# Performance work log

Measured on AMD Instinct MI355X. Metric: run time of the kernel, lower is better.

Reference implementation:

```python
import jax, jax.numpy as jnp
import numpy as np

N = 262144
D = 256
G = 2048

def setup_inputs() -> dict:
    key = jax.random.key(0)
    k1, k2, k3, k4, k5, k6 = jax.random.split(key, 6)
    x = jax.random.normal(k1, (N, D), dtype=jnp.float32)
    batch = jnp.sort(jax.random.randint(k2, (N,), 0, G, dtype=jnp.int32))
    # attention_net params: Linear(D, D//2) -> ReLU -> Linear(D//2, 1)
    s1 = 1.0 / np.sqrt(D)
    s2 = 1.0 / np.sqrt(D // 2)
    W1 = jax.random.uniform(k3, (D, D // 2), jnp.float32, -s1, s1)
    b1 = jax.random.uniform(k4, (D // 2,), jnp.float32, -s1, s1)
    W2 = jax.random.uniform(k5, (D // 2, 1), jnp.float32, -s2, s2)
    b2 = jax.random.uniform(k6, (1,), jnp.float32, -s2, s2)
    return {"x": x, "batch": batch, "num_graphs": G, "W1": W1, "b1": b1, "W2": W2, "b2": b2}

def reference(x, batch, num_graphs, W1, b1, W2, b2):
    # attention scores: [N, 1]
    h = jax.nn.relu(x @ W1 + b1)
    scores = (h @ W2 + b2)[:, 0]  # [N]
    # segment softmax over nodes of each graph (stable)
    seg_max = jax.ops.segment_max(scores, batch, num_segments=num_graphs)  # [G]
    ex = jnp.exp(scores - seg_max[batch])
    seg_sum = jax.ops.segment_sum(ex, batch, num_segments=num_graphs)  # [G]
    weights = ex / seg_sum[batch]  # [N]
    # weighted scatter-add pooling -> [G, D]
    graph_features = jax.ops.segment_sum(x * weights[:, None], batch, num_segments=num_graphs)
    return graph_features
```

## Files before the change

kernel.cpp:

```cpp
#include <hip/hip_runtime.h>
#include <hip/hip_bf16.h>

#define NN 262144
#define DD 256
#define HH 128
#define GG 2048

typedef __attribute__((ext_vector_type(8))) __bf16 bf16x8;
typedef __attribute__((ext_vector_type(4))) float f32x4;

union ABFrag { bf16x8 v; unsigned short u[8]; };
union BFrag  { bf16x8 v; uint4 i; };

__device__ __forceinline__ unsigned short f2bf(float f) {
    unsigned int u = __float_as_uint(f);
    unsigned int r = (u + 0x7fffu + ((u >> 16) & 1u)) >> 16;
    return (unsigned short)r;
}

__global__ void prep_kernel(const float* __restrict__ w1, unsigned short* __restrict__ w1t) {
    int i = blockIdx.x * 256 + threadIdx.x;
    int n = i >> 8;
    int k = i & 255;
    w1t[i] = f2bf(w1[k * HH + n]);
}

__global__ __launch_bounds__(256, 2)
void scores_kernel(const float* __restrict__ x,
                   const unsigned short* __restrict__ w1t,
                   const float* __restrict__ b1,
                   const float* __restrict__ w2,
                   const float* __restrict__ b2,
                   float* __restrict__ scores)
{
    const int lane = threadIdx.x & 63;
    const int wv   = threadIdx.x >> 6;
    const int c = lane & 15;
    const int q = lane >> 4;
    const int rowBlock = blockIdx.x * 256 + wv * 64;

    float b1v[8], w2v[8];
#pragma unroll
    for (int t = 0; t < 8; ++t) { b1v[t] = b1[t * 16 + c]; w2v[t] = w2[t * 16 + c]; }
    const float b2s = b2[0];

    f32x4 acc[4][8];
#pragma unroll
    for (int it = 0; it < 4; ++it)
#pragma unroll
        for (int t = 0; t < 8; ++t) acc[it][t] = (f32x4){0.f, 0.f, 0.f, 0.f};

#pragma unroll
    for (int kk = 0; kk < 8; ++kk) {
        BFrag bf[8];
#pragma unroll
        for (int t = 0; t < 8; ++t) {
            const uint4* p = (const uint4*)(w1t + (size_t)(t * 16 + c) * DD + kk * 32 + q * 8);
            bf[t].i = *p;
        }
#pragma unroll
        for (int it = 0; it < 4; ++it) {
            const float* px = x + (size_t)(rowBlock + it * 16 + c) * DD + kk * 32 + q * 8;
            float4 f0 = *(const float4*)px;
            float4 f1 = *(const float4*)(px + 4);
            ABFrag af;
            af.u[0] = f2bf(f0.x); af.u[1] = f2bf(f0.y); af.u[2] = f2bf(f0.z); af.u[3] = f2bf(f0.w);
            af.u[4] = f2bf(f1.x); af.u[5] = f2bf(f1.y); af.u[6] = f2bf(f1.z); af.u[7] = f2bf(f1.w);
#pragma unroll
            for (int t = 0; t < 8; ++t)
                acc[it][t] = __builtin_amdgcn_mfma_f32_16x16x32_bf16(af.v, bf[t].v, acc[it][t], 0, 0, 0);
        }
    }

#pragma unroll
    for (int it = 0; it < 4; ++it) {
        float s0 = 0.f, s1 = 0.f, s2 = 0.f, s3 = 0.f;
#pragma unroll
        for (int t = 0; t < 8; ++t) {
            float w = w2v[t], bb = b1v[t];
            f32x4 a = acc[it][t];
            s0 += fmaxf(a.x + bb, 0.f) * w;
            s1 += fmaxf(a.y + bb, 0.f) * w;
            s2 += fmaxf(a.z + bb, 0.f) * w;
            s3 += fmaxf(a.w + bb, 0.f) * w;
        }
#pragma unroll
        for (int off = 1; off < 16; off <<= 1) {
            s0 += __shfl_xor(s0, off);
            s1 += __shfl_xor(s1, off);
            s2 += __shfl_xor(s2, off);
            s3 += __shfl_xor(s3, off);
        }
        if (c == 0) {
            float* o = scores + rowBlock + it * 16 + q * 4;
            o[0] = s0 + b2s; o[1] = s1 + b2s; o[2] = s2 + b2s; o[3] = s3 + b2s;
        }
    }
}

__global__ void stats_kernel(const float* __restrict__ scores,
                             const int* __restrict__ batch,
                             float* __restrict__ gmax, float* __restrict__ ginv,
                             int* __restrict__ bstart, int* __restrict__ bend)
{
    int g = blockIdx.x;
    int lo = 0, hi = NN;
    while (lo < hi) { int mid = (lo + hi) >> 1; if (batch[mid] < g) lo = mid + 1; else hi = mid; }
    int start = lo;
    hi = NN;
    while (lo < hi) { int mid = (lo + hi) >> 1; if (batch[mid] < g + 1) lo = mid + 1; else hi = mid; }
    int end = lo;

    int lane = threadIdx.x;
    float m = -3.402823466e38f;
    for (int i = start + lane; i < end; i += 64) m = fmaxf(m, scores[i]);
#pragma unroll
    for (int off = 1; off < 64; off <<= 1) m = fmaxf(m, __shfl_xor(m, off));
    float sum = 0.f;
    for (int i = start + lane; i < end; i += 64) sum += __expf(scores[i] - m);
#pragma unroll
    for (int off = 1; off < 64; off <<= 1) sum += __shfl_xor(sum, off);
    if (lane == 0) {
        gmax[g] = m;
        ginv[g] = (end > start) ? 1.0f / sum : 0.0f;
        bstart[g] = start;
        bend[g] = end;
    }
}

__global__ __launch_bounds__(256)
void pool_kernel(const float* __restrict__ x, const float* __restrict__ scores,
                 const float* __restrict__ gmax, const float* __restrict__ ginv,
                 const int* __restrict__ bstart, const int* __restrict__ bend,
                 float* __restrict__ out)
{
    int g = blockIdx.x;
    int d = threadIdx.x;
    int start = bstart[g], end = bend[g];
    float m = gmax[g], inv = ginv[g];
    __shared__ float wl[256];
    float acc = 0.f;
    for (int base = start; base < end; base += 256) {
        int nch = min(256, end - base);
        __syncthreads();
        if (d < nch) wl[d] = __expf(scores[base + d] - m) * inv;
        __syncthreads();
        int j = 0;
        for (; j + 4 <= nch; j += 4) {
            const float* px = x + (size_t)(base + j) * DD + d;
            float x0 = px[0], x1 = px[DD], x2 = px[2 * DD], x3 = px[3 * DD];
            acc = fmaf(wl[j], x0, acc);
            acc = fmaf(wl[j + 1], x1, acc);
            acc = fmaf(wl[j + 2], x2, acc);
            acc = fmaf(wl[j + 3], x3, acc);
        }
        for (; j < nch; ++j) acc = fmaf(wl[j], x[(size_t)(base + j) * DD + d], acc);
    }
    out[(size_t)g * DD + d] = acc;
}

extern "C" void kernel_launch(void* const* d_in, const int* in_sizes, int n_in,
                              void* d_out, int out_size, void* d_ws, size_t ws_size,
                              hipStream_t stream) {
    const float* x     = (const float*)d_in[0];
    const int*   batch = (const int*)d_in[1];
    const float* W1    = (const float*)d_in[3];
    const float* b1    = (const float*)d_in[4];
    const float* W2    = (const float*)d_in[5];
    const float* b2    = (const float*)d_in[6];
    float* out = (float*)d_out;

    char* ws = (char*)d_ws;
    float*          scores = (float*)ws;
    unsigned short* w1t    = (unsigned short*)(ws + (size_t)NN * 4);
    float*          gmax   = (float*)(ws + (size_t)NN * 4 + 65536);
    float*          ginv   = gmax + GG;
    int*            bstart = (int*)(ginv + GG);
    int*            bend   = bstart + GG;

    prep_kernel<<<HH * DD / 256, 256, 0, stream>>>(W1, w1t);
    scores_kernel<<<NN / 256, 256, 0, stream>>>(x, w1t, b1, W2, b2, scores);
    stats_kernel<<<GG, 64, 0, stream>>>(scores, batch, gmax, ginv, bstart, bend);
    pool_kernel<<<GG, 256, 0, stream>>>(x, scores, gmax, ginv, bstart, bend, out);
}
```

Measured before the change: 433.5 us.

## Fuse score MLP, online segment softmax and pooling into one per-graph kernel

Replaces the separate scores, stats and pool kernels with a single kernel per graph. Each block stages W1 (bf16) in padded LDS, computes scores for 64-row chunks with MFMA, maintains an online softmax (running max and sum with rescaling), and accumulates the weighted pooling from the same rows, which are likely still in cache. Segment bounds come from a small separate binary-search kernel. This removes the scores round trip and the second full pass over x, but it adds three block barriers per 64-row chunk, lowers parallelism to one block per graph with about 68KB of LDS each, and repeats the W1 LDS load in every block. b2 is dropped because a constant shift cancels in the softmax.

```diff
diff --git a/kernel.cpp b/kernel.cpp
--- a/kernel.cpp
+++ b/kernel.cpp
@@ -5,17 +5,16 @@
 #define DD 256
 #define HH 128
 #define GG 2048
+#define LW1 264
 
 typedef __attribute__((ext_vector_type(8))) __bf16 bf16x8;
 typedef __attribute__((ext_vector_type(4))) float f32x4;
 
-union ABFrag { bf16x8 v; unsigned short u[8]; };
-union BFrag  { bf16x8 v; uint4 i; };
+union ABFrag { bf16x8 v; unsigned short u[8]; uint4 i; };
 
 __device__ __forceinline__ unsigned short f2bf(float f) {
     unsigned int u = __float_as_uint(f);
-    unsigned int r = (u + 0x7fffu + ((u >> 16) & 1u)) >> 16;
-    return (unsigned short)r;
+    return (unsigned short)((u + 0x7fffu + ((u >> 16) & 1u)) >> 16);
 }
 
 __global__ void prep_kernel(const float* __restrict__ w1, unsigned short* __restrict__ w1t) {
@@ -25,60 +24,88 @@
     w1t[i] = f2bf(w1[k * HH + n]);
 }
 
+__global__ void bounds_kernel(const int* __restrict__ batch, int* __restrict__ bnd) {
+    int g = blockIdx.x * 256 + threadIdx.x;
+    if (g > GG) return;
+    int lo = 0, hi = NN;
+    while (lo < hi) { int mid = (lo + hi) >> 1; if (batch[mid] < g) lo = mid + 1; else hi = mid; }
+    bnd[g] = lo;
+}
+
 __global__ __launch_bounds__(256, 2)
-void scores_kernel(const float* __restrict__ x,
-                   const unsigned short* __restrict__ w1t,
-                   const float* __restrict__ b1,
-                   const float* __restrict__ w2,
-                   const float* __restrict__ b2,
-                   float* __restrict__ scores)
+void fused_kernel(const float* __restrict__ x,
+                  const unsigned short* __restrict__ w1t,
+                  const float* __restrict__ b1,
+                  const float* __restrict__ w2,
+                  const int* __restrict__ bnd,
+                  float* __restrict__ out)
 {
-    const int lane = threadIdx.x & 63;
-    const int wv   = threadIdx.x >> 6;
+    __shared__ __align__(16) unsigned short w1s[HH * LW1];
+    __shared__ float s_lds[64];
+    __shared__ float e_lds[64];
+    __shared__ float bc[2];
+
+    const int g = blockIdx.x;
+    const int tid = threadIdx.x;
+    const int lane = tid & 63;
+    const int wv = tid >> 6;
     const int c = lane & 15;
     const int q = lane >> 4;
-    const int rowBlock = blockIdx.x * 256 + wv * 64;
+
+    const int start = bnd[g];
+    const int end = bnd[g + 1];
+
+#pragma unroll
+    for (int k = 0; k < 16; ++k) {
+        int idx = tid + k * 256;
+        int r = idx >> 5;
+        int col = (idx & 31) * 8;
+        *(uint4*)&w1s[r * LW1 + col] = ((const uint4*)w1t)[idx];
+    }
 
     float b1v[8], w2v[8];
 #pragma unroll
     for (int t = 0; t < 8; ++t) { b1v[t] = b1[t * 16 + c]; w2v[t] = w2[t * 16 + c]; }
-    const float b2s = b2[0];
 
-    f32x4 acc[4][8];
+    __syncthreads();
+
+    float acc = 0.f;
+    float m = -3.402823466e38f;
+    float l = 0.f;
+
+    for (int base = start; base < end; base += 64) {
+        f32x4 accs[8];
 #pragma unroll
-    for (int it = 0; it < 4; ++it)
-#pragma unroll
-        for (int t = 0; t < 8; ++t) acc[it][t] = (f32x4){0.f, 0.f, 0.f, 0.f};
+        for (int t = 0; t < 8; ++t) accs[t] = (f32x4){0.f, 0.f, 0.f, 0.f};
+
+        const int row = base + wv * 16 + c;
+        const bool valid = row < end;
+        const float* px = x + (size_t)row * DD;
 
 #pragma unroll
-    for (int kk = 0; kk < 8; ++kk) {
-        BFrag bf[8];
+        for (int kk = 0; kk < 8; ++kk) {
+            ABFrag af;
+            if (valid) {
+                float4 f0 = *(const float4*)(px + kk * 32 + q * 8);
+                float4 f1 = *(const float4*)(px + kk * 32 + q * 8 + 4);
+                af.u[0] = f2bf(f0.x); af.u[1] = f2bf(f0.y); af.u[2] = f2bf(f0.z); af.u[3] = f2bf(f0.w);
+                af.u[4] = f2bf(f1.x); af.u[5] = f2bf(f1.y); af.u[6] = f2bf(f1.z); af.u[7] = f2bf(f1.w);
+            } else {
+                af.i = (uint4){0u, 0u, 0u, 0u};
+            }
 #pragma unroll
-        for (int t = 0; t < 8; ++t) {
-            const uint4* p = (const uint4*)(w1t + (size_t)(t * 16 + c) * DD + kk * 32 + q * 8);
-            bf[t].i = *p;
+            for (int t = 0; t < 8; ++t) {
+                ABFrag bf;
+                bf.i = *(const uint4*)&w1s[(t * 16 + c) * LW1 + kk * 32 + q * 8];
+                accs[t] = __builtin_amdgcn_mfma_f32_16x16x32_bf16(af.v, bf.v, accs[t], 0, 0, 0);
+            }
         }
-#pragma unroll
-        for (int it = 0; it < 4; ++it) {
-            const float* px = x + (size_t)(rowBlock + it * 16 + c) * DD + kk * 32 + q * 8;
-            float4 f0 = *(const float4*)px;
-            float4 f1 = *(const float4*)(px + 4);
-            ABFrag af;
-            af.u[0] = f2bf(f0.x); af.u[1] = f2bf(f0.y); af.u[2] = f2bf(f0.z); af.u[3] = f2bf(f0.w);
-            af.u[4] = f2bf(f1.x); af.u[5] = f2bf(f1.y); af.u[6] = f2bf(f1.z); af.u[7] = f2bf(f1.w);
-#pragma unroll
-            for (int t = 0; t < 8; ++t)
-                acc[it][t] = __builtin_amdgcn_mfma_f32_16x16x32_bf16(af.v, bf[t].v, acc[it][t], 0, 0, 0);
-        }
-    }
 
-#pragma unroll
-    for (int it = 0; it < 4; ++it) {
         float s0 = 0.f, s1 = 0.f, s2 = 0.f, s3 = 0.f;
 #pragma unroll
         for (int t = 0; t < 8; ++t) {
             float w = w2v[t], bb = b1v[t];
-            f32x4 a = acc[it][t];
+            f32x4 a = accs[t];
             s0 += fmaxf(a.x + bb, 0.f) * w;
             s1 += fmaxf(a.y + bb, 0.f) * w;
             s2 += fmaxf(a.z + bb, 0.f) * w;
@@ -92,71 +119,45 @@
             s3 += __shfl_xor(s3, off);
         }
         if (c == 0) {
-            float* o = scores + rowBlock + it * 16 + q * 4;
-            o[0] = s0 + b2s; o[1] = s1 + b2s; o[2] = s2 + b2s; o[3] = s3 + b2s;
+            float* o = s_lds + wv * 16 + q * 4;
+            o[0] = s0; o[1] = s1; o[2] = s2; o[3] = s3;
         }
+        __syncthreads();
+
+        if (wv == 0) {
+            const int n = min(64, end - base);
+            float s = (lane < n) ? s_lds[lane] : -3.402823466e38f;
+            float cmax = s;
+#pragma unroll
+            for (int off = 1; off < 64; off <<= 1) cmax = fmaxf(cmax, __shfl_xor(cmax, off));
+            float newm = fmaxf(m, cmax);
+            float alpha = __expf(m - newm);
+            float e = (lane < n) ? __expf(s - newm) : 0.f;
+            float es = e;
+#pragma unroll
+            for (int off = 1; off < 64; off <<= 1) es += __shfl_xor(es, off);
+            l = l * alpha + es;
+            m = newm;
+            e_lds[lane] = e;
+            if (lane == 0) bc[0] = alpha;
+        }
+        __syncthreads();
+
+        const float alpha = bc[0];
+        acc *= alpha;
+        const int nn = min(64, NN - base);
+        const float* pxp = x + (size_t)base * DD + tid;
+#pragma unroll 8
+        for (int i = 0; i < nn; ++i) {
+            acc = fmaf(e_lds[i], pxp[(size_t)i * DD], acc);
+        }
+        __syncthreads();
     }
-}
 
-__global__ void stats_kernel(const float* __restrict__ scores,
-                             const int* __restrict__ batch,
-                             float* __restrict__ gmax, float* __restrict__ ginv,
-                             int* __restrict__ bstart, int* __restrict__ bend)
-{
-    int g = blockIdx.x;
-    int lo = 0, hi = NN;
-    while (lo < hi) { int mid = (lo + hi) >> 1; if (batch[mid] < g) lo = mid + 1; else hi = mid; }
-    int start = lo;
-    hi = NN;
-    while (lo < hi) { int mid = (lo + hi) >> 1; if (batch[mid] < g + 1) lo = mid + 1; else hi = mid; }
-    int end = lo;
-
-    int lane = threadIdx.x;
-    float m = -3.402823466e38f;
-    for (int i = start + lane; i < end; i += 64) m = fmaxf(m, scores[i]);
-#pragma unroll
-    for (int off = 1; off < 64; off <<= 1) m = fmaxf(m, __shfl_xor(m, off));
-    float sum = 0.f;
-    for (int i = start + lane; i < end; i += 64) sum += __expf(scores[i] - m);
-#pragma unroll
-    for (int off = 1; off < 64; off <<= 1) sum += __shfl_xor(sum, off);
-    if (lane == 0) {
-        gmax[g] = m;
-        ginv[g] = (end > start) ? 1.0f / sum : 0.0f;
-        bstart[g] = start;
-        bend[g] = end;
-    }
-}
-
-__global__ __launch_bounds__(256)
-void pool_kernel(const float* __restrict__ x, const float* __restrict__ scores,
-                 const float* __restrict__ gmax, const float* __restrict__ ginv,
-                 const int* __restrict__ bstart, const int* __restrict__ bend,
-                 float* __restrict__ out)
-{
-    int g = blockIdx.x;
-    int d = threadIdx.x;
-    int start = bstart[g], end = bend[g];
-    float m = gmax[g], inv = ginv[g];
-    __shared__ float wl[256];
-    float acc = 0.f;
-    for (int base = start; base < end; base += 256) {
-        int nch = min(256, end - base);
-        __syncthreads();
-        if (d < nch) wl[d] = __expf(scores[base + d] - m) * inv;
-        __syncthreads();
-        int j = 0;
-        for (; j + 4 <= nch; j += 4) {
-            const float* px = x + (size_t)(base + j) * DD + d;
-            float x0 = px[0], x1 = px[DD], x2 = px[2 * DD], x3 = px[3 * DD];
-            acc = fmaf(wl[j], x0, acc);
-            acc = fmaf(wl[j + 1], x1, acc);
-            acc = fmaf(wl[j + 2], x2, acc);
-            acc = fmaf(wl[j + 3], x3, acc);
-        }
-        for (; j < nch; ++j) acc = fmaf(wl[j], x[(size_t)(base + j) * DD + d], acc);
-    }
-    out[(size_t)g * DD + d] = acc;
+    if (wv == 0 && lane == 0) bc[1] = l;
+    __syncthreads();
+    const float L = bc[1];
+    out[(size_t)g * DD + tid] = (L > 0.f) ? acc / L : 0.f;
 }
 
 extern "C" void kernel_launch(void* const* d_in, const int* in_sizes, int n_in,
@@ -167,19 +168,13 @@
     const float* W1    = (const float*)d_in[3];
     const float* b1    = (const float*)d_in[4];
     const float* W2    = (const float*)d_in[5];
-    const float* b2    = (const float*)d_in[6];
     float* out = (float*)d_out;
 
     char* ws = (char*)d_ws;
-    float*          scores = (float*)ws;
-    unsigned short* w1t    = (unsigned short*)(ws + (size_t)NN * 4);
-    float*          gmax   = (float*)(ws + (size_t)NN * 4 + 65536);
-    float*          ginv   = gmax + GG;
-    int*            bstart = (int*)(ginv + GG);
-    int*            bend   = bstart + GG;
+    unsigned short* w1t = (unsigned short*)ws;
+    int*            bnd = (int*)(ws + 65536);
 
     prep_kernel<<<HH * DD / 256, 256, 0, stream>>>(W1, w1t);
-    scores_kernel<<<NN / 256, 256, 0, stream>>>(x, w1t, b1, W2, b2, scores);
-    stats_kernel<<<GG, 64, 0, stream>>>(scores, batch, gmax, ginv, bstart, bend);
-    pool_kernel<<<GG, 256, 0, stream>>>(x, scores, gmax, ginv, bstart, bend, out);
+    bounds_kernel<<<(GG + 1 + 255) / 256, 256, 0, stream>>>(batch, bnd);
+    fused_kernel<<<GG, 256, 0, stream>>>(x, w1t, b1, W2, bnd, out);
 }
```

New measurement: 444.9 us. 2.6% more time.
